# Kernel tuning notes

Hardware: AMD Instinct MI355X
Metric: run time of the kernel (lower is better)

The kernel has to match this reference:

```python
import jax, jax.numpy as jnp
import numpy as np


def setup_inputs() -> dict:
    key = jax.random.key(0)
    k0, k1, k2, k3 = jax.random.split(key, 4)
    B, N, C = 4, 1024, 64
    x = jax.random.normal(k0, (B, N, C), dtype=jnp.float32)
    # torch nn.Linear weights are [out, in]; all projections are bias-free
    W1 = jax.random.normal(k1, (C, C), dtype=jnp.float32) * (1.0 / np.sqrt(C))
    W2 = jax.random.normal(k2, (C, C), dtype=jnp.float32) * (1.0 / np.sqrt(C))
    w3 = jax.random.normal(k3, (C,), dtype=jnp.float32) * (1.0 / np.sqrt(C))
    return {"x": x, "W1": W1, "W2": W2, "w3": w3}


def reference(x, W1, W2, w3):
    # x: [B, N, C]; torch Linear: y = x @ W.T
    x1 = jnp.einsum("bnc,dc->bnd", x, W1)  # [B, N, C]
    x2 = jnp.einsum("bnc,dc->bnd", x, W2)  # [B, N, C]
    # broadcast-add over node pairs, tanh, project C -> 1: [B, N, N]
    combined = jnp.tanh(x1[:, :, None, :] + x2[:, None, :, :])  # [B, N, N, C]
    att = jnp.einsum("bijc,c->bij", combined, w3)
    return jax.nn.softmax(att, axis=-1)
```

## Files before the change

### kernel.cpp

```cpp
#include <hip/hip_runtime.h>
#include <hip/hip_bf16.h>


#define BATCH 4
#define NN    1024
#define CC    64
#define TI    4
#define BLK   256
#define PP    65
#define PROWS 16

__device__ __forceinline__ float fast_exp2(float x) {
#if __has_builtin(__builtin_amdgcn_exp2f)
    return __builtin_amdgcn_exp2f(x);
#else
    return exp2f(x);
#endif
}
__device__ __forceinline__ float fast_rcp(float x) {
#if __has_builtin(__builtin_amdgcn_rcpf)
    return __builtin_amdgcn_rcpf(x);
#else
    return 1.0f / x;
#endif
}

__global__ __launch_bounds__(512) void proj_kernel(
    const float* __restrict__ x, const float* __restrict__ W1,
    const float* __restrict__ W2, float* __restrict__ e1p,
    float* __restrict__ e2p) {
    __shared__ float w1t[CC * PP];
    __shared__ float w2t[CC * PP];
    __shared__ float xs[PROWS * CC];

    const int tid = threadIdx.x;
    const int r0  = blockIdx.x * PROWS;
    {
        const float4* __restrict__ W1v = (const float4*)W1;
        const float4* __restrict__ W2v = (const float4*)W2;
#pragma unroll
        for (int k = 0; k < 2; ++k) {
            const int fi = k * 512 + tid;
            const int r  = fi >> 4;
            const int c4 = (fi & 15) * 4;
            float4 a = W1v[fi], b = W2v[fi];
            w1t[(c4 + 0) * PP + r] = a.x; w1t[(c4 + 1) * PP + r] = a.y;
            w1t[(c4 + 2) * PP + r] = a.z; w1t[(c4 + 3) * PP + r] = a.w;
            w2t[(c4 + 0) * PP + r] = b.x; w2t[(c4 + 1) * PP + r] = b.y;
            w2t[(c4 + 2) * PP + r] = b.z; w2t[(c4 + 3) * PP + r] = b.w;
        }
        const int rr = tid >> 6, c = tid & 63;
#pragma unroll
        for (int k = 0; k < 2; ++k) {
            const int r = k * 8 + rr;
            xs[r * CC + c] = x[(size_t)(r0 + r) * CC + c];
        }
    }
    __syncthreads();

    const int w    = tid >> 6;
    const int lane = tid & 63;
    const int rb   = w * 2;

    float a1[2] = {0.f, 0.f};
    float a2[2] = {0.f, 0.f};
#pragma unroll
    for (int c = 0; c < CC; ++c) {
        const float w1v = w1t[c * PP + lane];
        const float w2v = w2t[c * PP + lane];
        const float x0 = xs[(rb + 0) * CC + c];
        const float x1 = xs[(rb + 1) * CC + c];
        a1[0] = fmaf(x0, w1v, a1[0]);  a2[0] = fmaf(x0, w2v, a2[0]);
        a1[1] = fmaf(x1, w1v, a1[1]);  a2[1] = fmaf(x1, w2v, a2[1]);
    }
    const float K2 = 2.8853900817779268f;
#pragma unroll
    for (int rr = 0; rr < 2; ++rr) {
        const size_t r = (size_t)(r0 + rb + rr);
        e1p[r * CC + lane] = fast_exp2(fminf(a1[rr] * K2, 15.f));
    }
    {
        const int b  = r0 >> 10;
        const int n0 = r0 & 1023;
        const int cq = lane >> 2, cm = lane & 3;
        const size_t base =
            ((((size_t)(b * 16 + cq)) << 10) + (size_t)(n0 + rb)) * 4 + cm;
#pragma unroll
        for (int rr = 0; rr < 2; ++rr) {
            e2p[base + (size_t)rr * 4] = fast_exp2(fminf(a2[rr] * K2, 15.f));
        }
    }
}

__device__ __forceinline__ void step2(float e1a, float e1b, float e2,
                                      float wc, float2& acc) {
    float da = fmaf(e1a, e2, 1.f);
    float db = fmaf(e1b, e2, 1.f);
    float r  = fast_rcp(da * db);
    float t  = wc * r;
    acc.x = fmaf(db, t, acc.x);
    acc.y = fmaf(da, t, acc.y);
}

__global__ __launch_bounds__(BLK) void attn_kernel(
    const float* __restrict__ e1p, const float* __restrict__ e2p,
    const float* __restrict__ w3, float* __restrict__ out) {
    __shared__ float e1t[CC * TI];
    __shared__ float att_lds[TI * NN];

    const int tid = threadIdx.x;
    const int bi  = blockIdx.x;
    const int b   = bi >> 8;
    const int i0  = (bi & 255) * TI;

    {
        const int ii = tid >> 6, c = tid & 63;
        e1t[c * TI + ii] = e1p[(size_t)((b << 10) + i0 + ii) * CC + c];
    }
    __syncthreads();

    const float4* __restrict__ w3q = (const float4*)w3;
    float sumw3 = 0.f;
#pragma unroll
    for (int q = 0; q < 16; ++q) {
        float4 t = w3q[q];
        sumw3 += (t.x + t.y) + (t.z + t.w);
    }

    const float4* __restrict__ e2b4 = ((const float4*)e2p) + ((size_t)b << 14);
    const float4* e1t4 = (const float4*)e1t;

#pragma unroll 1
    for (int ch = 0; ch < 2; ++ch) {
        const int jA = (ch << 8) + tid;
        const int jB = jA + 512;

        float2 accA1 = {0.f, 0.f}, accB1 = {0.f, 0.f};
        float2 accA2 = {0.f, 0.f}, accB2 = {0.f, 0.f};

#pragma unroll 1
        for (int ct = 0; ct < 4; ++ct) {
            float4 La[4], Lb[4];
#pragma unroll
            for (int q = 0; q < 4; ++q) {
                const int cq = ct * 4 + q;
                La[q] = e2b4[(cq << 10) + jA];
                Lb[q] = e2b4[(cq << 10) + jB];
            }
#pragma unroll
            for (int q = 0; q < 4; ++q) {
                const int cq = ct * 4 + q;
                const float4 wv  = w3q[cq];
                const float eA[4] = {La[q].x, La[q].y, La[q].z, La[q].w};
                const float eB[4] = {Lb[q].x, Lb[q].y, Lb[q].z, Lb[q].w};
                const float wa[4] = {wv.x, wv.y, wv.z, wv.w};
#pragma unroll
                for (int m = 0; m < 4; ++m) {
                    const int c = cq * 4 + m;
                    const float4 ev = e1t4[c];
                    step2(ev.x, ev.y, eA[m], wa[m], accA1);
                    step2(ev.z, ev.w, eA[m], wa[m], accB1);
                    step2(ev.x, ev.y, eB[m], wa[m], accA2);
                    step2(ev.z, ev.w, eB[m], wa[m], accB2);
                }
            }
        }
        att_lds[0 * NN + jA] = fmaf(-2.f, accA1.x, sumw3);
        att_lds[1 * NN + jA] = fmaf(-2.f, accA1.y, sumw3);
        att_lds[2 * NN + jA] = fmaf(-2.f, accB1.x, sumw3);
        att_lds[3 * NN + jA] = fmaf(-2.f, accB1.y, sumw3);
        att_lds[0 * NN + jB] = fmaf(-2.f, accA2.x, sumw3);
        att_lds[1 * NN + jB] = fmaf(-2.f, accA2.y, sumw3);
        att_lds[2 * NN + jB] = fmaf(-2.f, accB2.x, sumw3);
        att_lds[3 * NN + jB] = fmaf(-2.f, accB2.y, sumw3);
    }
    __syncthreads();

    {
        const int w    = tid >> 6;
        const int lane = tid & 63;
        float v[16];
        float m = -3.4e38f;
#pragma unroll
        for (int k = 0; k < 16; ++k) {
            v[k] = att_lds[w * NN + k * 64 + lane];
            m = fmaxf(m, v[k]);
        }
#pragma unroll
        for (int off = 32; off >= 1; off >>= 1)
            m = fmaxf(m, __shfl_xor(m, off));
        const float L2E = 1.4426950408889634f;
        float s = 0.f;
#pragma unroll
        for (int k = 0; k < 16; ++k) {
            v[k] = fast_exp2((v[k] - m) * L2E);
            s += v[k];
        }
#pragma unroll
        for (int off = 32; off >= 1; off >>= 1)
            s += __shfl_xor(s, off);
        const float rs = fast_rcp(s);
        float* __restrict__ orow = out + (((size_t)(b << 10) + (i0 + w)) << 10);
#pragma unroll
        for (int k = 0; k < 16; ++k) orow[k * 64 + lane] = v[k] * rs;
    }
}

extern "C" void kernel_launch(void* const* d_in, const int* in_sizes, int n_in,
                              void* d_out, int out_size, void* d_ws, size_t ws_size,
                              hipStream_t stream) {
    const float* x  = (const float*)d_in[0];
    const float* W1 = (const float*)d_in[1];
    const float* W2 = (const float*)d_in[2];
    const float* w3 = (const float*)d_in[3];
    float* outp = (float*)d_out;

    float* e1p = (float*)d_ws;
    float* e2p = e1p + (size_t)BATCH * NN * CC;

    proj_kernel<<<dim3(BATCH * NN / PROWS), dim3(512), 0, stream>>>(x, W1, W2, e1p, e2p);
    attn_kernel<<<dim3(BATCH * NN / TI), dim3(BLK), 0, stream>>>(e1p, e2p, w3, outp);
}
```

Baseline: 95.84 us.

## Process all four j columns per thread in one pass, stage w3 in LDS

Each thread now covers its four j columns in a single pass over the channels, dropping the outer two-chunk loop. This halves how often the e1 tile and w3 are reread from LDS and global memory per output. w3 is copied into shared memory, and launch bounds request four blocks per CU to steer register allocation. In exchange each thread holds more accumulators and loaded values, which may raise register pressure or cut the latency hiding from back-to-back loads.

```diff
diff --git a/kernel.cpp b/kernel.cpp
--- a/kernel.cpp
+++ b/kernel.cpp
@@ -102,10 +102,11 @@
     acc.y = fmaf(da, t, acc.y);
 }
 
-__global__ __launch_bounds__(BLK) void attn_kernel(
+__global__ __launch_bounds__(BLK, 4) void attn_kernel(
     const float* __restrict__ e1p, const float* __restrict__ e2p,
     const float* __restrict__ w3, float* __restrict__ out) {
     __shared__ float e1t[CC * TI];
+    __shared__ float w3s[CC];
     __shared__ float att_lds[TI * NN];
 
     const int tid = threadIdx.x;
@@ -117,7 +118,7 @@
         const int ii = tid >> 6, c = tid & 63;
         e1t[c * TI + ii] = e1p[(size_t)((b << 10) + i0 + ii) * CC + c];
     }
-    __syncthreads();
+    if (tid < CC) w3s[tid] = w3[tid];
 
     const float4* __restrict__ w3q = (const float4*)w3;
     float sumw3 = 0.f;
@@ -127,52 +128,52 @@
         sumw3 += (t.x + t.y) + (t.z + t.w);
     }
 
+    __syncthreads();
+
+    const float4* e1t4 = (const float4*)e1t;
+    const float4* w3s4 = (const float4*)w3s;
     const float4* __restrict__ e2b4 = ((const float4*)e2p) + ((size_t)b << 14);
-    const float4* e1t4 = (const float4*)e1t;
+
+    float2 acc[4][2];
+#pragma unroll
+    for (int jj = 0; jj < 4; ++jj) {
+        acc[jj][0] = make_float2(0.f, 0.f);
+        acc[jj][1] = make_float2(0.f, 0.f);
+    }
 
 #pragma unroll 1
-    for (int ch = 0; ch < 2; ++ch) {
-        const int jA = (ch << 8) + tid;
-        const int jB = jA + 512;
-
-        float2 accA1 = {0.f, 0.f}, accB1 = {0.f, 0.f};
-        float2 accA2 = {0.f, 0.f}, accB2 = {0.f, 0.f};
-
-#pragma unroll 1
-        for (int ct = 0; ct < 4; ++ct) {
-            float4 La[4], Lb[4];
-#pragma unroll
-            for (int q = 0; q < 4; ++q) {
-                const int cq = ct * 4 + q;
-                La[q] = e2b4[(cq << 10) + jA];
-                Lb[q] = e2b4[(cq << 10) + jB];
-            }
-#pragma unroll
-            for (int q = 0; q < 4; ++q) {
-                const int cq = ct * 4 + q;
-                const float4 wv  = w3q[cq];
-                const float eA[4] = {La[q].x, La[q].y, La[q].z, La[q].w};
-                const float eB[4] = {Lb[q].x, Lb[q].y, Lb[q].z, Lb[q].w};
-                const float wa[4] = {wv.x, wv.y, wv.z, wv.w};
-#pragma unroll
-                for (int m = 0; m < 4; ++m) {
-                    const int c = cq * 4 + m;
-                    const float4 ev = e1t4[c];
-                    step2(ev.x, ev.y, eA[m], wa[m], accA1);
-                    step2(ev.z, ev.w, eA[m], wa[m], accB1);
-                    step2(ev.x, ev.y, eB[m], wa[m], accA2);
-                    step2(ev.z, ev.w, eB[m], wa[m], accB2);
+    for (int ct = 0; ct < 4; ++ct) {
+#pragma unroll
+        for (int q = 0; q < 4; ++q) {
+            const int cq = ct * 4 + q;
+            float4 L[4];
+#pragma unroll
+            for (int jj = 0; jj < 4; ++jj)
+                L[jj] = e2b4[(cq << 10) + tid + (jj << 8)];
+            const float4 wv = w3s4[cq];
+#pragma unroll
+            for (int m = 0; m < 4; ++m) {
+                const float4 ev = e1t4[cq * 4 + m];
+                const float wc = (m == 0) ? wv.x : (m == 1) ? wv.y
+                               : (m == 2) ? wv.z : wv.w;
+#pragma unroll
+                for (int jj = 0; jj < 4; ++jj) {
+                    const float e2v = (m == 0) ? L[jj].x : (m == 1) ? L[jj].y
+                                    : (m == 2) ? L[jj].z : L[jj].w;
+                    step2(ev.x, ev.y, e2v, wc, acc[jj][0]);
+                    step2(ev.z, ev.w, e2v, wc, acc[jj][1]);
                 }
             }
         }
-        att_lds[0 * NN + jA] = fmaf(-2.f, accA1.x, sumw3);
-        att_lds[1 * NN + jA] = fmaf(-2.f, accA1.y, sumw3);
-        att_lds[2 * NN + jA] = fmaf(-2.f, accB1.x, sumw3);
-        att_lds[3 * NN + jA] = fmaf(-2.f, accB1.y, sumw3);
-        att_lds[0 * NN + jB] = fmaf(-2.f, accA2.x, sumw3);
-        att_lds[1 * NN + jB] = fmaf(-2.f, accA2.y, sumw3);
-        att_lds[2 * NN + jB] = fmaf(-2.f, accB2.x, sumw3);
-        att_lds[3 * NN + jB] = fmaf(-2.f, accB2.y, sumw3);
+    }
+
+#pragma unroll
+    for (int jj = 0; jj < 4; ++jj) {
+        const int j = tid + (jj << 8);
+        att_lds[0 * NN + j] = fmaf(-2.f, acc[jj][0].x, sumw3);
+        att_lds[1 * NN + j] = fmaf(-2.f, acc[jj][0].y, sumw3);
+        att_lds[2 * NN + j] = fmaf(-2.f, acc[jj][1].x, sumw3);
+        att_lds[3 * NN + j] = fmaf(-2.f, acc[jj][1].y, sumw3);
     }
     __syncthreads();
 
```

Measured after the change: 104.6 us. +9.2%, slower.
